# Optimization experiments

Hardware: AMD Instinct MI355X
Metric: run time of the kernel (lower is better)

Reference implementation:

```python
import jax, jax.numpy as jnp
import numpy as np

N_HEAD = 16
ROPE_BASE = 10000.0


def setup_inputs() -> dict:
    key = jax.random.key(0)
    k1, k2, k3 = jax.random.split(key, 3)
    B, N, C = 2, 2048, 2048
    x = jax.random.normal(k1, (B, N, C), dtype=jnp.float32)
    position_ids = jnp.tile(jnp.arange(N, dtype=jnp.int64)[None, :], (B, 1))
    # torch nn.Linear(d, 3d) weight is [3d, d]; we store the transposed [d, 3d] for x @ W
    Wqkv = jax.random.normal(k2, (C, 3 * C), dtype=jnp.float32) * (C ** -0.5)
    Wproj = jax.random.normal(k3, (C, C), dtype=jnp.float32) * (C ** -0.5)
    return {"x": x, "position_ids": position_ids, "Wqkv": Wqkv, "Wproj": Wproj}


def _rotate_half(t):
    d = t.shape[-1] // 2
    return jnp.concatenate([-t[..., d:], t[..., :d]], axis=-1)


def reference(x, position_ids, Wqkv, Wproj):
    B, N, C = x.shape
    H = N_HEAD
    hd = C // H
    scale = hd ** -0.5

    # fused QKV projection -> [3, B, H, N, hd]
    qkv = (x @ Wqkv).reshape(B, N, 3, H, hd).transpose(2, 0, 3, 1, 4)
    q, k, v = qkv[0], qkv[1], qkv[2]

    # RoPE (computed in fp32 as in the original)
    inv_freq = 1.0 / (ROPE_BASE ** (jnp.arange(0, hd, 2, dtype=jnp.float32) / hd))
    freqs = position_ids.astype(jnp.float32)[:, :, None] * inv_freq[None, None, :]  # [B, N, hd/2]
    emb = jnp.concatenate([freqs, freqs], axis=-1)                                  # [B, N, hd]
    cos = jnp.cos(emb)[:, None, :, :].astype(x.dtype)  # [B, 1, N, hd]
    sin = jnp.sin(emb)[:, None, :, :].astype(x.dtype)
    q = q * cos + _rotate_half(q) * sin
    k = k * cos + _rotate_half(k) * sin

    # causal SDPA
    scores = jnp.einsum('bhqd,bhkd->bhqk', q, k) * scale
    causal = jnp.tril(jnp.ones((N, N), dtype=bool))
    scores = jnp.where(causal[None, None, :, :], scores, jnp.finfo(scores.dtype).min)
    attn = jax.nn.softmax(scores, axis=-1)
    out = jnp.einsum('bhqk,bhkd->bhqd', attn, v)

    out = out.transpose(0, 2, 1, 3).reshape(B, N, C)
    return out @ Wproj
```

## Files before the change

### kernel.cpp

```cpp
#include <hip/hip_runtime.h>
#include <stdint.h>

#define DEV __device__ __forceinline__

typedef __attribute__((ext_vector_type(8))) short short8;
typedef __attribute__((ext_vector_type(8))) unsigned short ushort8;
typedef __attribute__((ext_vector_type(4))) float f32x4;
typedef __attribute__((ext_vector_type(16))) float f32x16;
typedef __attribute__((ext_vector_type(2))) unsigned int uint2v;

DEV unsigned short f2bf(float f) {
  union { float f; uint32_t u; } v; v.f = f;
  uint32_t u = v.u;
  u += 0x7FFFu + ((u >> 16) & 1);
  return (unsigned short)(u >> 16);
}
DEV float bf2f(unsigned short s) {
  union { uint32_t u; float f; } v; v.u = ((uint32_t)s) << 16;
  return v.f;
}
DEV float exp2_fast(float x) {
  float r; asm("v_exp_f32 %0, %1" : "=v"(r) : "v"(x)); return r;
}
DEV uint32_t cvt_pk_bf16(float lo, float hi) {
  uint32_t r; asm("v_cvt_pk_bf16_f32 %0, %1, %2" : "=v"(r) : "v"(lo), "v"(hi)); return r;
}

DEV void async_ld16(void* lds, const void* g) {
  __builtin_amdgcn_global_load_lds(
      (const __attribute__((address_space(1))) unsigned int*)g,
      (__attribute__((address_space(3))) unsigned int*)lds, 16, 0, 0);
}

__global__ __launch_bounds__(256) void cast_bf16_kernel(
    const float* __restrict__ in, unsigned short* __restrict__ out, int n) {
  int i = (blockIdx.x * 256 + threadIdx.x) * 4;
  if (i >= n) return;
  f32x4 v = *(const f32x4*)(in + i);
  union { unsigned short u[4]; uint2v v2; } o;
#pragma unroll
  for (int j = 0; j < 4; ++j) o.u[j] = f2bf(v[j]);
  *(uint2v*)(out + i) = o.v2;
}

__global__ __launch_bounds__(256) void transpose_cast_kernel(
    const float* __restrict__ in, unsigned short* __restrict__ out, int R, int C) {
  __shared__ float tile[32][33];
  const int c0 = blockIdx.x * 32, r0 = blockIdx.y * 32;
  const int tx = threadIdx.x & 31, ty = threadIdx.x >> 5;
#pragma unroll
  for (int i = 0; i < 32; i += 8)
    tile[ty + i][tx] = in[(size_t)(r0 + ty + i) * C + c0 + tx];
  __syncthreads();
#pragma unroll
  for (int i = 0; i < 32; i += 8)
    out[(size_t)(c0 + ty + i) * R + r0 + tx] = f2bf(tile[tx][ty + i]);
}

template <int OUT_BF16>
__global__ __launch_bounds__(512, 2) void gemm_bt64(
    const unsigned short* __restrict__ A, const unsigned short* __restrict__ Bt,
    void* __restrict__ Cout, int M, int Nn, int K) {
  __shared__ unsigned short As[2][256 * 64];
  __shared__ unsigned short Bs[2][128 * 64];
  const int t = threadIdx.x;
  const int lane = t & 63, w = t >> 6;
  const int wr = (w >> 1) * 64;
  const int wc = (w & 1) * 64;
  const int brow = blockIdx.y * 256, bcol = blockIdx.x * 128;
  const int l15 = lane & 15, lk = lane >> 4;
  const int p = l15 & 7;

  f32x4 acc[4][4] = {};

  auto stage = [&](int buf, int ktile) {
    const int koff = ktile * 64;
#pragma unroll
    for (int j = 0; j < 4; ++j) {
      const int slot = j * 512 + t;
      const int row = slot >> 3, ch = slot & 7;
      const int sc = ch ^ (row & 7);
      async_ld16(&As[buf][slot * 8], A + (size_t)(brow + row) * K + koff + sc * 8);
    }
#pragma unroll
    for (int j = 0; j < 2; ++j) {
      const int slot = j * 512 + t;
      const int row = slot >> 3, ch = slot & 7;
      const int sc = ch ^ (row & 7);
      async_ld16(&Bs[buf][slot * 8], Bt + (size_t)(bcol + row) * K + koff + sc * 8);
    }
  };

  const int NT = K / 64;
  stage(0, 0);
  stage(1, 1);

  for (int kt = 0; kt < NT; ++kt) {
    const int cur = kt & 1;
    if (kt == NT - 1) { asm volatile("s_waitcnt vmcnt(0)" ::: "memory"); }
    else              { asm volatile("s_waitcnt vmcnt(6)" ::: "memory"); }
    __builtin_amdgcn_sched_barrier(0);
    __builtin_amdgcn_s_barrier();

    short8 af0[4], af1[4], bf0[4], bf1[4];
#pragma unroll
    for (int m = 0; m < 4; ++m) {
      const int row = wr + m * 16 + l15;
      af0[m] = *(const short8*)&As[cur][row * 64 + (lk ^ p) * 8];
      af1[m] = *(const short8*)&As[cur][row * 64 + ((4 + lk) ^ p) * 8];
    }
#pragma unroll
    for (int n = 0; n < 4; ++n) {
      const int row = wc + n * 16 + l15;
      bf0[n] = *(const short8*)&Bs[cur][row * 64 + (lk ^ p) * 8];
      bf1[n] = *(const short8*)&Bs[cur][row * 64 + ((4 + lk) ^ p) * 8];
    }

    __builtin_amdgcn_s_setprio(1);
#pragma unroll
    for (int m = 0; m < 4; ++m)
#pragma unroll
      for (int n = 0; n < 4; ++n)
        acc[m][n] = __builtin_amdgcn_mfma_f32_16x16x32_bf16(af0[m], bf0[n], acc[m][n], 0, 0, 0);
    __builtin_amdgcn_s_setprio(0);

    asm volatile("s_waitcnt lgkmcnt(0)" ::: "memory");
    __builtin_amdgcn_sched_barrier(0);
    __builtin_amdgcn_s_barrier();
    if (kt + 2 < NT) stage(cur, kt + 2);

    __builtin_amdgcn_s_setprio(1);
#pragma unroll
    for (int m = 0; m < 4; ++m)
#pragma unroll
      for (int n = 0; n < 4; ++n)
        acc[m][n] = __builtin_amdgcn_mfma_f32_16x16x32_bf16(af1[m], bf1[n], acc[m][n], 0, 0, 0);
    __builtin_amdgcn_s_setprio(0);
  }

#pragma unroll
  for (int m = 0; m < 4; ++m)
#pragma unroll
    for (int n = 0; n < 4; ++n)
#pragma unroll
      for (int j = 0; j < 4; ++j) {
        const int row = brow + wr + m * 16 + lk * 4 + j;
        const int col = bcol + wc + n * 16 + l15;
        if (OUT_BF16)
          ((unsigned short*)Cout)[(size_t)row * Nn + col] = f2bf(acc[m][n][j]);
        else
          ((float*)Cout)[(size_t)row * Nn + col] = acc[m][n][j];
      }
}

template <int OUT_BF16>
__global__ __launch_bounds__(512, 2) void gemm_bt32(
    const unsigned short* __restrict__ A, const unsigned short* __restrict__ Bt,
    void* __restrict__ Cout, int M, int Nn, int K) {
  __shared__ unsigned short As[2][256 * 32];
  __shared__ unsigned short Bs[2][128 * 32];
  const int t = threadIdx.x;
  const int lane = t & 63, w = t >> 6;
  const int wr = (w >> 1) * 64;
  const int wc = (w & 1) * 64;
  const int brow = blockIdx.y * 256, bcol = blockIdx.x * 128;
  const int l15 = lane & 15, lk = lane >> 4;

  f32x4 acc[4][4] = {};

  auto stage = [&](int buf, int ktile) {
    const int koff = ktile * 32;
#pragma unroll
    for (int j = 0; j < 2; ++j) {
      const int slot = j * 512 + t;
      const int row = slot >> 2, ch = slot & 3;
      const int sc = ch ^ ((row >> 1) & 3);
      async_ld16(&As[buf][slot * 8], A + (size_t)(brow + row) * K + koff + sc * 8);
    }
    {
      const int slot = t;
      const int row = slot >> 2, ch = slot & 3;
      const int sc = ch ^ ((row >> 1) & 3);
      async_ld16(&Bs[buf][slot * 8], Bt + (size_t)(bcol + row) * K + koff + sc * 8);
    }
  };

  const int NT = K / 32;
  stage(0, 0);
  stage(1, 1);

  for (int kt = 0; kt < NT; ++kt) {
    const int cur = kt & 1;
    if (kt == NT - 1) { asm volatile("s_waitcnt vmcnt(0)" ::: "memory"); }
    else              { asm volatile("s_waitcnt vmcnt(3)" ::: "memory"); }
    __builtin_amdgcn_sched_barrier(0);
    __builtin_amdgcn_s_barrier();

    short8 af0[4], bf0[4];
#pragma unroll
    for (int m = 0; m < 4; ++m) {
      const int row = wr + m * 16 + l15;
      af0[m] = *(const short8*)&As[cur][row * 32 + (lk ^ ((row >> 1) & 3)) * 8];
    }
#pragma unroll
    for (int n = 0; n < 4; ++n) {
      const int row = wc + n * 16 + l15;
      bf0[n] = *(const short8*)&Bs[cur][row * 32 + (lk ^ ((row >> 1) & 3)) * 8];
    }

    __builtin_amdgcn_s_setprio(1);
#pragma unroll
    for (int m = 0; m < 4; ++m)
#pragma unroll
      for (int n = 0; n < 4; ++n)
        acc[m][n] = __builtin_amdgcn_mfma_f32_16x16x32_bf16(af0[m], bf0[n], acc[m][n], 0, 0, 0);
    __builtin_amdgcn_s_setprio(0);

    asm volatile("s_waitcnt lgkmcnt(0)" ::: "memory");
    __builtin_amdgcn_sched_barrier(0);
    __builtin_amdgcn_s_barrier();
    if (kt + 2 < NT) stage(cur, kt + 2);
  }

#pragma unroll
  for (int m = 0; m < 4; ++m)
#pragma unroll
    for (int n = 0; n < 4; ++n)
#pragma unroll
      for (int j = 0; j < 4; ++j) {
        const int row = brow + wr + m * 16 + lk * 4 + j;
        const int col = bcol + wc + n * 16 + l15;
        if (OUT_BF16)
          ((unsigned short*)Cout)[(size_t)row * Nn + col] = f2bf(acc[m][n][j]);
        else
          ((float*)Cout)[(size_t)row * Nn + col] = acc[m][n][j];
      }
}

#define QSCALE 0.12751743f
__global__ __launch_bounds__(256) void rope_pack(
    const unsigned short* __restrict__ Y, const int* __restrict__ pos,
    unsigned short* __restrict__ Qb, unsigned short* __restrict__ Kb,
    unsigned short* __restrict__ Vt, int N) {
  __shared__ unsigned short vt[128 * 32];
  const int bh = blockIdx.x, b = bh >> 4, h = bh & 15;
  const int n0 = blockIdx.y * 32;
  const int t = threadIdx.x;
  const int tok = t >> 3, dp0 = (t & 7) * 8;
  const int n = n0 + tok;
  const float p = (float)pos[b * N + n];
  const size_t yb = (size_t)(b * N + n) * 6144 + h * 128;

  ushort8 qlo = *(const ushort8*)&Y[yb + dp0];
  ushort8 qhi = *(const ushort8*)&Y[yb + dp0 + 64];
  ushort8 klo = *(const ushort8*)&Y[yb + 2048 + dp0];
  ushort8 khi = *(const ushort8*)&Y[yb + 2048 + dp0 + 64];
  ushort8 vlo = *(const ushort8*)&Y[yb + 4096 + dp0];
  ushort8 vhi = *(const ushort8*)&Y[yb + 4096 + dp0 + 64];

  ushort8 oql, oqh, okl, okh;
#pragma unroll
  for (int i = 0; i < 8; ++i) {
    const float d = (float)(dp0 + i);
    const float ang = p * exp2f(d * -0.2076205059304601f);
    const float s = sinf(ang), c = cosf(ang);
    const float ql = bf2f(qlo[i]), qh = bf2f(qhi[i]);
    const float kl = bf2f(klo[i]), kh = bf2f(khi[i]);
    oql[i] = f2bf((ql * c - qh * s) * QSCALE);
    oqh[i] = f2bf((qh * c + ql * s) * QSCALE);
    okl[i] = f2bf(kl * c - kh * s);
    okh[i] = f2bf(kh * c + kl * s);
    vt[(dp0 + i) * 32 + tok] = vlo[i];
    vt[(dp0 + 64 + i) * 32 + tok] = vhi[i];
  }
  const size_t qb = ((size_t)bh * N + n) * 128;
  *(ushort8*)&Qb[qb + dp0] = oql;
  *(ushort8*)&Qb[qb + dp0 + 64] = oqh;
  *(ushort8*)&Kb[qb + dp0] = okl;
  *(ushort8*)&Kb[qb + dp0 + 64] = okh;
  __syncthreads();
  const int d = t >> 1, half = t & 1;
  const size_t vdst = (size_t)bh * 128 * N + (size_t)d * N + n0 + half * 16;
  *(ushort8*)&Vt[vdst]     = *(const ushort8*)&vt[d * 32 + half * 16];
  *(ushort8*)&Vt[vdst + 8] = *(const ushort8*)&vt[d * 32 + half * 16 + 8];
}

__global__ __launch_bounds__(256, 2) void flash_attn4(
    const unsigned short* __restrict__ Qb, const unsigned short* __restrict__ Kb,
    const unsigned short* __restrict__ Vt, unsigned short* __restrict__ Ao, int N) {
  __shared__ unsigned short Ks[2][32 * 128];
  __shared__ unsigned short Vs[2][128 * 32];
  const int t = threadIdx.x, lane = t & 63, w = t >> 6;
  const int bh = blockIdx.x, b = bh >> 4, h = bh & 15;
  const int y = blockIdx.y;
  const int cc = (y < 8) ? (15 - y) : (y - 8);
  const int q0 = cc * 128 + w * 32;
  const int l31 = lane & 31, hi = lane >> 5;
  const size_t base = (size_t)bh * N * 128;
  const size_t vbase = (size_t)bh * 128 * N;
  const int Twave = 4 * cc + w;
  const int Tblk = 4 * cc + 4;

  auto stage = [&](int tt, int buf) {
    const int kv0 = tt * 32;
#pragma unroll
    for (int j = 0; j < 2; ++j) {
      const int slot = j * 256 + t;
      const int krow = slot >> 4, kch = (slot & 15) ^ (krow & 7);
      async_ld16(&Ks[buf][slot * 8], Kb + base + (size_t)(kv0 + krow) * 128 + kch * 8);
    }
#pragma unroll
    for (int j = 0; j < 2; ++j) {
      const int slot = j * 256 + t;
      const int vrow = slot >> 2, vch = (slot & 3) ^ (vrow & 3);
      async_ld16(&Vs[buf][slot * 8], Vt + vbase + (size_t)vrow * N + kv0 + vch * 8);
    }
  };

  short8 qf[8];
#pragma unroll
  for (int s = 0; s < 8; ++s)
    qf[s] = *(const short8*)&Qb[base + (size_t)(q0 + l31) * 128 + s * 16 + hi * 8];

  f32x16 acc0 = {}, acc1 = {}, acc2 = {}, acc3 = {};
  float m_run = -1e30f, l_run = 0.f;

  stage(0, 0);
  stage(1, 1);

  for (int tt = 0; tt < Tblk; ++tt) {
    const int cur = tt & 1;
    if (tt < Tblk - 1) { asm volatile("s_waitcnt vmcnt(4)" ::: "memory"); }
    else               { asm volatile("s_waitcnt vmcnt(0)" ::: "memory"); }
    __builtin_amdgcn_sched_barrier(0);
    __builtin_amdgcn_s_barrier();

    if (tt <= Twave) {
      const int kv0 = tt * 32;
      const bool masked = (tt == Twave);

      short8 kf[8];
#pragma unroll
      for (int s = 0; s < 8; ++s)
        kf[s] = *(const short8*)&Ks[cur][l31 * 128 + ((2 * s + hi) ^ (l31 & 7)) * 8];
      short8 vf[8];
#pragma unroll
      for (int c2 = 0; c2 < 2; ++c2)
#pragma unroll
        for (int dblk = 0; dblk < 4; ++dblk) {
          const int row = dblk * 32 + l31;
          vf[c2 * 4 + dblk] = *(const short8*)&Vs[cur][row * 32 + ((2 * c2 + hi) ^ (row & 3)) * 8];
        }

      f32x16 st = {};
      __builtin_amdgcn_s_setprio(1);
#pragma unroll
      for (int s = 0; s < 8; ++s)
        st = __builtin_amdgcn_mfma_f32_32x32x16_bf16(kf[s], qf[s], st, 0, 0, 0);
      __builtin_amdgcn_s_setprio(0);

      if (masked) {
        const int qg = q0 + l31;
#pragma unroll
        for (int r = 0; r < 16; ++r) {
          const int kvg = kv0 + (r & 3) + 8 * ((r >> 2) & 1) + 16 * (r >> 3) + 4 * hi;
          st[r] = (kvg > qg) ? -1e30f : st[r];
        }
      }
      float a0 = fmaxf(st[0], st[1]),  a1 = fmaxf(st[2], st[3]),
            a2 = fmaxf(st[4], st[5]),  a3 = fmaxf(st[6], st[7]),
            a4 = fmaxf(st[8], st[9]),  a5 = fmaxf(st[10], st[11]),
            a6 = fmaxf(st[12], st[13]), a7 = fmaxf(st[14], st[15]);
      a0 = fmaxf(a0, a1); a2 = fmaxf(a2, a3); a4 = fmaxf(a4, a5); a6 = fmaxf(a6, a7);
      a0 = fmaxf(a0, a2); a4 = fmaxf(a4, a6);
      float mt = fmaxf(a0, a4);
      mt = fmaxf(mt, __shfl_xor(mt, 32));

      float m_new = fmaxf(m_run, mt);
      const bool defer = __all(mt - m_run <= 8.f);
      if (defer) {
        m_new = m_run;
      } else {
        const float alpha = exp2_fast(m_run - m_new);
        l_run *= alpha;
#pragma unroll
        for (int r = 0; r < 16; ++r) {
          acc0[r] *= alpha; acc1[r] *= alpha; acc2[r] *= alpha; acc3[r] *= alpha;
        }
      }
      m_run = m_new;

#pragma unroll
      for (int r = 0; r < 16; ++r) st[r] = exp2_fast(st[r] - m_new);
      float s0 = (st[0] + st[1]) + (st[2] + st[3]), s1 = (st[4] + st[5]) + (st[6] + st[7]);
      float s2 = (st[8] + st[9]) + (st[10] + st[11]), s3 = (st[12] + st[13]) + (st[14] + st[15]);
      float lsum = (s0 + s1) + (s2 + s3);
      lsum += __shfl_xor(lsum, 32);
      l_run += lsum;

      short8 pB0, pB1;
#pragma unroll
      for (int c2 = 0; c2 < 2; ++c2) {
        const int o = c2 * 8;
        const uint32_t P01 = cvt_pk_bf16(st[o + 0], st[o + 1]);
        const uint32_t P23 = cvt_pk_bf16(st[o + 2], st[o + 3]);
        const uint32_t P45 = cvt_pk_bf16(st[o + 4], st[o + 5]);
        const uint32_t P67 = cvt_pk_bf16(st[o + 6], st[o + 7]);
        const uint32_t S01 = (uint32_t)__shfl_xor((int)P01, 32);
        const uint32_t S23 = (uint32_t)__shfl_xor((int)P23, 32);
        const uint32_t S45 = (uint32_t)__shfl_xor((int)P45, 32);
        const uint32_t S67 = (uint32_t)__shfl_xor((int)P67, 32);
        union { uint32_t ww[4]; short8 s8; } u;
        u.ww[0] = hi ? S45 : P01;
        u.ww[1] = hi ? S67 : P23;
        u.ww[2] = hi ? P45 : S01;
        u.ww[3] = hi ? P67 : S23;
        if (c2 == 0) pB0 = u.s8; else pB1 = u.s8;
      }

      __builtin_amdgcn_s_setprio(1);
      acc0 = __builtin_amdgcn_mfma_f32_32x32x16_bf16(vf[0], pB0, acc0, 0, 0, 0);
      acc1 = __builtin_amdgcn_mfma_f32_32x32x16_bf16(vf[1], pB0, acc1, 0, 0, 0);
      acc2 = __builtin_amdgcn_mfma_f32_32x32x16_bf16(vf[2], pB0, acc2, 0, 0, 0);
      acc3 = __builtin_amdgcn_mfma_f32_32x32x16_bf16(vf[3], pB0, acc3, 0, 0, 0);
      acc0 = __builtin_amdgcn_mfma_f32_32x32x16_bf16(vf[4], pB1, acc0, 0, 0, 0);
      acc1 = __builtin_amdgcn_mfma_f32_32x32x16_bf16(vf[5], pB1, acc1, 0, 0, 0);
      acc2 = __builtin_amdgcn_mfma_f32_32x32x16_bf16(vf[6], pB1, acc2, 0, 0, 0);
      acc3 = __builtin_amdgcn_mfma_f32_32x32x16_bf16(vf[7], pB1, acc3, 0, 0, 0);
      __builtin_amdgcn_s_setprio(0);
    }

    asm volatile("s_waitcnt lgkmcnt(0)" ::: "memory");
    __builtin_amdgcn_sched_barrier(0);
    __builtin_amdgcn_s_barrier();
    if (tt + 2 < Tblk) stage(tt + 2, cur);
  }

  const float inv = 1.f / l_run;
  const size_t orow = (size_t)(b * N + q0 + l31) * 2048 + h * 128;
#pragma unroll
  for (int r = 0; r < 16; r += 2) {
    const int doff = (r & 3) + 8 * ((r >> 2) & 1) + 16 * (r >> 3) + 4 * hi;
    *(uint32_t*)&Ao[orow + 0  + doff] = cvt_pk_bf16(acc0[r] * inv, acc0[r + 1] * inv);
    *(uint32_t*)&Ao[orow + 32 + doff] = cvt_pk_bf16(acc1[r] * inv, acc1[r + 1] * inv);
    *(uint32_t*)&Ao[orow + 64 + doff] = cvt_pk_bf16(acc2[r] * inv, acc2[r + 1] * inv);
    *(uint32_t*)&Ao[orow + 96 + doff] = cvt_pk_bf16(acc3[r] * inv, acc3[r + 1] * inv);
  }
}

extern "C" void kernel_launch(void* const* d_in, const int* in_sizes, int n_in,
                              void* d_out, int out_size, void* d_ws, size_t ws_size,
                              hipStream_t stream) {
  const float* x      = (const float*)d_in[0];
  const int*   pos    = (const int*)d_in[1];
  const float* Wqkv   = (const float*)d_in[2];
  const float* Wproj  = (const float*)d_in[3];
  float* out = (float*)d_out;

  const int N = 2048, C = 2048;
  const int M = 2 * N;

  char* ws = (char*)d_ws;
  unsigned short* Xb      = (unsigned short*)(ws + 0);
  unsigned short* Wqkv_t  = (unsigned short*)(ws + 16777216);
  unsigned short* Wproj_t = (unsigned short*)(ws + 41943040);
  unsigned short* Y       = (unsigned short*)(ws + 50331648);
  unsigned short* Qb      = (unsigned short*)(ws + 100663296);
  unsigned short* Kb      = (unsigned short*)(ws + 117440512);
  unsigned short* Vt      = (unsigned short*)(ws + 134217728);
  unsigned short* Ao = Xb;

  cast_bf16_kernel<<<(M * C) / 1024, 256, 0, stream>>>(x, Xb, M * C);
  transpose_cast_kernel<<<dim3(3 * C / 32, C / 32), 256, 0, stream>>>(Wqkv, Wqkv_t, C, 3 * C);
  transpose_cast_kernel<<<dim3(C / 32, C / 32), 256, 0, stream>>>(Wproj, Wproj_t, C, C);
  gemm_bt32<1><<<dim3(3 * C / 128, M / 256), 512, 0, stream>>>(Xb, Wqkv_t, Y, M, 3 * C, C);
  rope_pack<<<dim3(32, N / 32), 256, 0, stream>>>(Y, pos, Qb, Kb, Vt, N);
  flash_attn4<<<dim3(32, 16), 256, 0, stream>>>(Qb, Kb, Vt, Ao, N);
  gemm_bt64<0><<<dim3(C / 128, M / 256), 512, 0, stream>>>(Ao, Wproj_t, out, M, C, C);
}
```

Before: 299.9 us.

## Fuse RoPE and Q/K/V repacking into the QKV GEMM epilogue

The QKV projection GEMM now applies RoPE, the Q scale and the head-major or transposed-V layout directly in its epilogue, staging through LDS. This removes the bf16 Y intermediate and the separate rope_pack pass. The GEMM also moves to a 64-wide K tile with the second half of the MFMAs issued after the next stage's loads. A small kernel precomputes cos/sin tables indexed by position, which are read in the epilogue. LDS use rises to 96KB per block, which may limit occupancy.

Result: faster. 265.4 us (-11.5%).

```diff
diff --git a/kernel.cpp b/kernel.cpp
--- a/kernel.cpp
+++ b/kernel.cpp
@@ -31,6 +31,8 @@
       (const __attribute__((address_space(1))) unsigned int*)g,
       (__attribute__((address_space(3))) unsigned int*)lds, 16, 0, 0);
 }
+
+#define QSCALE 0.12751743f
 
 __global__ __launch_bounds__(256) void cast_bf16_kernel(
     const float* __restrict__ in, unsigned short* __restrict__ out, int n) {
@@ -55,6 +57,15 @@
 #pragma unroll
   for (int i = 0; i < 32; i += 8)
     out[(size_t)(c0 + ty + i) * R + r0 + tx] = f2bf(tile[tx][ty + i]);
+}
+
+__global__ __launch_bounds__(256) void rope_table(
+    float* __restrict__ cosT, float* __restrict__ sinT) {
+  const int i = blockIdx.x * 256 + threadIdx.x;
+  const int n = i >> 6, d = i & 63;
+  const float ang = (float)n * exp2f((float)d * -0.2076205059304601f);
+  cosT[i] = cosf(ang);
+  sinT[i] = sinf(ang);
 }
 
 template <int OUT_BF16>
@@ -153,59 +164,66 @@
       }
 }
 
-template <int OUT_BF16>
-__global__ __launch_bounds__(512, 2) void gemm_bt32(
+__global__ __launch_bounds__(512, 2) void gemm_qkv_rope(
     const unsigned short* __restrict__ A, const unsigned short* __restrict__ Bt,
-    void* __restrict__ Cout, int M, int Nn, int K) {
-  __shared__ unsigned short As[2][256 * 32];
-  __shared__ unsigned short Bs[2][128 * 32];
+    const int* __restrict__ pos, const float* __restrict__ cosT,
+    const float* __restrict__ sinT, unsigned short* __restrict__ Qb,
+    unsigned short* __restrict__ Kb, unsigned short* __restrict__ Vt,
+    int M, int Nn, int K) {
+  __shared__ unsigned short smem[49152];
+  unsigned short* As = smem;
+  unsigned short* Bs = smem + 32768;
   const int t = threadIdx.x;
   const int lane = t & 63, w = t >> 6;
   const int wr = (w >> 1) * 64;
   const int wc = (w & 1) * 64;
   const int brow = blockIdx.y * 256, bcol = blockIdx.x * 128;
   const int l15 = lane & 15, lk = lane >> 4;
+  const int p = l15 & 7;
 
   f32x4 acc[4][4] = {};
 
   auto stage = [&](int buf, int ktile) {
-    const int koff = ktile * 32;
+    const int koff = ktile * 64;
+#pragma unroll
+    for (int j = 0; j < 4; ++j) {
+      const int slot = j * 512 + t;
+      const int row = slot >> 3, ch = slot & 7;
+      const int sc = ch ^ (row & 7);
+      async_ld16(&As[buf * 16384 + slot * 8], A + (size_t)(brow + row) * K + koff + sc * 8);
+    }
 #pragma unroll
     for (int j = 0; j < 2; ++j) {
       const int slot = j * 512 + t;
-      const int row = slot >> 2, ch = slot & 3;
-      const int sc = ch ^ ((row >> 1) & 3);
-      async_ld16(&As[buf][slot * 8], A + (size_t)(brow + row) * K + koff + sc * 8);
-    }
-    {
-      const int slot = t;
-      const int row = slot >> 2, ch = slot & 3;
-      const int sc = ch ^ ((row >> 1) & 3);
-      async_ld16(&Bs[buf][slot * 8], Bt + (size_t)(bcol + row) * K + koff + sc * 8);
+      const int row = slot >> 3, ch = slot & 7;
+      const int sc = ch ^ (row & 7);
+      async_ld16(&Bs[buf * 8192 + slot * 8], Bt + (size_t)(bcol + row) * K + koff + sc * 8);
     }
   };
 
-  const int NT = K / 32;
+  const int NT = K / 64;
   stage(0, 0);
   stage(1, 1);
 
   for (int kt = 0; kt < NT; ++kt) {
     const int cur = kt & 1;
     if (kt == NT - 1) { asm volatile("s_waitcnt vmcnt(0)" ::: "memory"); }
-    else              { asm volatile("s_waitcnt vmcnt(3)" ::: "memory"); }
+    else              { asm volatile("s_waitcnt vmcnt(6)" ::: "memory"); }
     __builtin_amdgcn_sched_barrier(0);
     __builtin_amdgcn_s_barrier();
 
-    short8 af0[4], bf0[4];
+    short8 af0[4], af1[4], bf0[4], bf1[4];
 #pragma unroll
     for (int m = 0; m < 4; ++m) {
       const int row = wr + m * 16 + l15;
-      af0[m] = *(const short8*)&As[cur][row * 32 + (lk ^ ((row >> 1) & 3)) * 8];
+      af0[m] = *(const short8*)&As[cur * 16384 + row * 64 + (lk ^ p) * 8];
+      af1[m] = *(const short8*)&As[cur * 16384 + row * 64 + ((4 + lk) ^ p) * 8];
     }
 #pragma unroll
     for (int n = 0; n < 4; ++n) {
       const int row = wc + n * 16 + l15;
-      bf0[n] = *(const short8*)&Bs[cur][row * 32 + (lk ^ ((row >> 1) & 3)) * 8];
+      bf0[n] = *(const short8*)&Bs[cur * 8192 + row * 64 + (lk ^ p) * 8];
+      bf1[n] = *(const short8*)&Bs[cur * 8192 + row * 64 + ((4 + lk) ^ p) * 8];
     }
 
     __builtin_amdgcn_s_setprio(1);
@@ -220,69 +238,92 @@
     __builtin_amdgcn_sched_barrier(0);
     __builtin_amdgcn_s_barrier();
     if (kt + 2 < NT) stage(cur, kt + 2);
+
+    __builtin_amdgcn_s_setprio(1);
+#pragma unroll
+    for (int m = 0; m < 4; ++m)
+#pragma unroll
+      for (int n = 0; n < 4; ++n)
+        acc[m][n] = __builtin_amdgcn_mfma_f32_16x16x32_bf16(af1[m], bf1[n], acc[m][n], 0, 0, 0);
+    __builtin_amdgcn_s_setprio(0);
   }
 
-#pragma unroll
-  for (int m = 0; m < 4; ++m)
-#pragma unroll
-    for (int n = 0; n < 4; ++n)
-#pragma unroll
-      for (int j = 0; j < 4; ++j) {
-        const int row = brow + wr + m * 16 + lk * 4 + j;
-        const int col = bcol + wc + n * 16 + l15;
-        if (OUT_BF16)
-          ((unsigned short*)Cout)[(size_t)row * Nn + col] = f2bf(acc[m][n][j]);
-        else
-          ((float*)Cout)[(size_t)row * Nn + col] = acc[m][n][j];
-      }
-}
-
-#define QSCALE 0.12751743f
-__global__ __launch_bounds__(256) void rope_pack(
-    const unsigned short* __restrict__ Y, const int* __restrict__ pos,
-    unsigned short* __restrict__ Qb, unsigned short* __restrict__ Kb,
-    unsigned short* __restrict__ Vt, int N) {
-  __shared__ unsigned short vt[128 * 32];
-  const int bh = blockIdx.x, b = bh >> 4, h = bh & 15;
-  const int n0 = blockIdx.y * 32;
-  const int t = threadIdx.x;
-  const int tok = t >> 3, dp0 = (t & 7) * 8;
-  const int n = n0 + tok;
-  const float p = (float)pos[b * N + n];
-  const size_t yb = (size_t)(b * N + n) * 6144 + h * 128;
-
-  ushort8 qlo = *(const ushort8*)&Y[yb + dp0];
-  ushort8 qhi = *(const ushort8*)&Y[yb + dp0 + 64];
-  ushort8 klo = *(const ushort8*)&Y[yb + 2048 + dp0];
-  ushort8 khi = *(const ushort8*)&Y[yb + 2048 + dp0 + 64];
-  ushort8 vlo = *(const ushort8*)&Y[yb + 4096 + dp0];
-  ushort8 vhi = *(const ushort8*)&Y[yb + 4096 + dp0 + 64];
-
-  ushort8 oql, oqh, okl, okh;
-#pragma unroll
-  for (int i = 0; i < 8; ++i) {
-    const float d = (float)(dp0 + i);
-    const float ang = p * exp2f(d * -0.2076205059304601f);
-    const float s = sinf(ang), c = cosf(ang);
-    const float ql = bf2f(qlo[i]), qh = bf2f(qhi[i]);
-    const float kl = bf2f(klo[i]), kh = bf2f(khi[i]);
-    oql[i] = f2bf((ql * c - qh * s) * QSCALE);
-    oqh[i] = f2bf((qh * c + ql * s) * QSCALE);
-    okl[i] = f2bf(kl * c - kh * s);
-    okh[i] = f2bf(kh * c + kl * s);
-    vt[(dp0 + i) * 32 + tok] = vlo[i];
-    vt[(dp0 + 64 + i) * 32 + tok] = vhi[i];
+  __syncthreads();
+
+  const int mode = bcol >> 11;
+  const int h = (bcol >> 7) & 15;
+  const int b = brow >> 11, n0 = brow & 2047;
+
+  if (mode == 2) {
+#pragma unroll
+    for (int m = 0; m < 4; ++m)
+#pragma unroll
+      for (int n = 0; n < 4; ++n) {
+        const int d = wc + n * 16 + l15;
+        const int tok = wr + m * 16 + lk * 4;
+        union { unsigned short u[4]; uint2v v2; } pk;
+#pragma unroll
+        for (int j = 0; j < 4; ++j) pk.u[j] = f2bf(acc[m][n][j]);
+        *(uint2v*)&smem[d * 264 + tok] = pk.v2;
+      }
+    __syncthreads();
+    const size_t vbase = (size_t)(b * 16 + h) * 128 * 2048;
+    const int half = t >> 5, l32 = t & 31;
+#pragma unroll
+    for (int pp = 0; pp < 8; ++pp) {
+      const int d = pp * 16 + half;
+      const int nl = l32 * 8;
+      ushort8 v = *(const ushort8*)&smem[d * 264 + nl];
+      *(ushort8*)&Vt[vbase + (size_t)d * 2048 + n0 + nl] = v;
+    }
+  } else {
+    const float sc = (mode == 0) ? QSCALE : 1.0f;
+#pragma unroll
+    for (int m = 0; m < 4; ++m)
+#pragma unroll
+      for (int n = 0; n < 4; ++n) {
+        const int d = wc + n * 16 + l15;
+#pragma unroll
+        for (int j = 0; j < 4; ++j) {
+          const int r = wr + m * 16 + lk * 4 + j;
+          smem[r * 136 + d] = f2bf(acc[m][n][j] * sc);
+        }
+      }
+    __syncthreads();
+    unsigned short* dst = (mode == 0) ? Qb : Kb;
+    const int d0 = (t & 7) * 8;
+#pragma unroll
+    for (int pass = 0; pass < 4; ++pass) {
+      const int r = pass * 64 + (t >> 3);
+      const int prow = brow + r;
+      const int pi = pos[prow];
+      const short8 lo8 = *(const short8*)&smem[r * 136 + d0];
+      const short8 hi8 = *(const short8*)&smem[r * 136 + 64 + d0];
+      const f32x4 c0 = *(const f32x4*)&cosT[pi * 64 + d0];
+      const f32x4 c1 = *(const f32x4*)&cosT[pi * 64 + d0 + 4];
+      const f32x4 s0 = *(const f32x4*)&sinT[pi * 64 + d0];
+      const f32x4 s1 = *(const f32x4*)&sinT[pi * 64 + d0 + 4];
+      float olo[8], ohi[8];
+#pragma unroll
+      for (int i = 0; i < 8; ++i) {
+        const float lo = bf2f((unsigned short)lo8[i]);
+        const float hi = bf2f((unsigned short)hi8[i]);
+        const float c = (i < 4) ? c0[i & 3] : c1[i & 3];
+        const float s = (i < 4) ? s0[i & 3] : s1[i & 3];
+        olo[i] = lo * c - hi * s;
+        ohi[i] = hi * c + lo * s;
+      }
+      union { uint32_t w4[4]; ushort8 s8; } ulo, uhi;
+#pragma unroll
+      for (int k = 0; k < 4; ++k) {
+        ulo.w4[k] = cvt_pk_bf16(olo[2 * k], olo[2 * k + 1]);
+        uhi.w4[k] = cvt_pk_bf16(ohi[2 * k], ohi[2 * k + 1]);
+      }
+      const size_t base = ((size_t)((prow >> 11) * 16 + h) * 2048 + (prow & 2047)) * 128;
+      *(ushort8*)&dst[base + d0] = ulo.s8;
+      *(ushort8*)&dst[base + 64 + d0] = uhi.s8;
+    }
   }
-  const size_t qb = ((size_t)bh * N + n) * 128;
-  *(ushort8*)&Qb[qb + dp0] = oql;
-  *(ushort8*)&Qb[qb + dp0 + 64] = oqh;
-  *(ushort8*)&Kb[qb + dp0] = okl;
-  *(ushort8*)&Kb[qb + dp0 + 64] = okh;
-  __syncthreads();
-  const int d = t >> 1, half = t & 1;
-  const size_t vdst = (size_t)bh * 128 * N + (size_t)d * N + n0 + half * 16;
-  *(ushort8*)&Vt[vdst]     = *(const ushort8*)&vt[d * 32 + half * 16];
-  *(ushort8*)&Vt[vdst + 8] = *(const ushort8*)&vt[d * 32 + half * 16 + 8];
 }
 
 __global__ __launch_bounds__(256, 2) void flash_attn4(
@@ -464,7 +505,8 @@
   unsigned short* Xb      = (unsigned short*)(ws + 0);
   unsigned short* Wqkv_t  = (unsigned short*)(ws + 16777216);
   unsigned short* Wproj_t = (unsigned short*)(ws + 41943040);
-  unsigned short* Y       = (unsigned short*)(ws + 50331648);
+  float*          cosT    = (float*)(ws + 50331648);
+  float*          sinT    = (float*)(ws + 50855936);
   unsigned short* Qb      = (unsigned short*)(ws + 100663296);
   unsigned short* Kb      = (unsigned short*)(ws + 117440512);
   unsigned short* Vt      = (unsigned short*)(ws + 134217728);
@@ -473,8 +515,9 @@
   cast_bf16_kernel<<<(M * C) / 1024, 256, 0, stream>>>(x, Xb, M * C);
   transpose_cast_kernel<<<dim3(3 * C / 32, C / 32), 256, 0, stream>>>(Wqkv, Wqkv_t, C, 3 * C);
   transpose_cast_kernel<<<dim3(C / 32, C / 32), 256, 0, stream>>>(Wproj, Wproj_t, C, C);
-  gemm_bt32<1><<<dim3(3 * C / 128, M / 256), 512, 0, stream>>>(Xb, Wqkv_t, Y, M, 3 * C, C);
-  rope_pack<<<dim3(32, N / 32), 256, 0, stream>>>(Y, pos, Qb, Kb, Vt, N);
+  rope_table<<<512, 256, 0, stream>>>(cosT, sinT);
+  gemm_qkv_rope<<<dim3(3 * C / 128, M / 256), 512, 0, stream>>>(
+      Xb, Wqkv_t, pos, cosT, sinT, Qb, Kb, Vt, M, 3 * C, C);
   flash_attn4<<<dim3(32, 16), 256, 0, stream>>>(Qb, Kb, Vt, Ao, N);
   gemm_bt64<0><<<dim3(C / 128, M / 256), 512, 0, stream>>>(Ao, Wproj_t, out, M, C, C);
 }
```
